# Performance work log

Hardware: AMD Instinct MI355X
Metric: run time of the kernel (lower is better)

The kernel has to match this reference:

```python
import jax, jax.numpy as jnp
import numpy as np

N, F = 4096, 255          # nodes, raw feature dim (one-hot adds +1 -> 256)
HID, D = 256, 256         # GCN hidden and out_dim
B, T, G = 8, 16384, 4     # n_breakings, n_tuples, n_groups
LN_EPS = 1e-5


def setup_inputs() -> dict:
    key = jax.random.key(0)
    ks = jax.random.split(key, 8)
    X = jax.random.normal(ks[0], (N, F), jnp.float32)
    adj_t = jax.random.uniform(ks[1], (N, N), jnp.float32)  # dense weighted adjacency
    W1 = jax.random.normal(ks[2], (F + 1, HID), jnp.float32) * 0.05
    b1 = jnp.zeros((HID,), jnp.float32)
    W2 = jax.random.normal(ks[3], (HID, D), jnp.float32) * 0.05
    b2 = jnp.zeros((D,), jnp.float32)
    ln_gamma = jnp.ones((D,), jnp.float32)
    ln_beta = jnp.zeros((D,), jnp.float32)
    tuples_coo = jax.random.randint(ks[4], (2, T), 0, N)
    group_idx = jax.random.randint(ks[5], (B,), 0, G)
    return dict(X=X, adj_t=adj_t, W1=W1, b1=b1, W2=W2, b2=b2,
                ln_gamma=ln_gamma, ln_beta=ln_beta,
                tuples_coo=tuples_coo, group_idx=group_idx,
                n_breakings=B, n_groups=G)


def reference(X, adj_t, W1, b1, W2, b2, ln_gamma, ln_beta,
              tuples_coo, group_idx, n_breakings, n_groups):
    n = X.shape[0]
    # --- symmetry breaking: top-k degree nodes (ties improbable for float degrees) ---
    deg = adj_t.sum(-1)                                   # [N]
    _, brk_idx = jax.lax.top_k(deg, n_breakings)          # [B]
    one_hot = jax.nn.one_hot(brk_idx, n, dtype=X.dtype)   # [B, N]
    # --- concat broadcast features with one-hot breaking channel ---
    Xin = jnp.concatenate(
        [jnp.broadcast_to(X[None], (n_breakings,) + X.shape), one_hot[..., None]],
        axis=-1)                                          # [B, N, F+1]
    # --- symmetry_breaking_model: 2-layer dense-adjacency GCN ---
    h = jax.nn.relu(jnp.einsum('nm,bmf->bnf', adj_t, Xin) @ W1 + b1)   # [B, N, HID]
    out = jnp.einsum('nm,bmf->bnf', adj_t, h) @ W2 + b2                # [B, N, D]
    # --- LayerNorm over feature dim ---
    mu = out.mean(-1, keepdims=True)
    var = out.var(-1, keepdims=True)
    holo = (out - mu) * jax.lax.rsqrt(var + LN_EPS) * ln_gamma + ln_beta  # [B, N, D]
    # --- gather tuple endpoints and reduce by product over arity ---
    gathered = holo[:, tuples_coo]                        # [B, arity, T, D]
    set_repr = gathered.prod(axis=1)                      # [B, T, D]
    # --- scatter-mean over breakings by group ---
    sums = jax.ops.segment_sum(set_repr, group_idx, num_segments=n_groups)  # [G, T, D]
    counts = jax.ops.segment_sum(jnp.ones((set_repr.shape[0],), set_repr.dtype),
                                 group_idx, num_segments=n_groups)          # [G]
    link = sums / jnp.maximum(counts, 1.0)[:, None, None]  # [G, T, D]
    # transpose(0,1).flatten(1,2): [T, G*D]
    return jnp.transpose(link, (1, 0, 2)).reshape(link.shape[1], -1)
```

## Files before the change

### kernel.cpp

```cpp
#include <hip/hip_runtime.h>
#include <hip/hip_bf16.h>

#define N_NODES 4096
#define FEAT    255
#define NB      8
#define NT      16384
#define NG      4

typedef __attribute__((ext_vector_type(8))) short          short8;
typedef __attribute__((ext_vector_type(8))) __bf16         bf16x8;
typedef __attribute__((ext_vector_type(4))) float          f32x4;
typedef __attribute__((ext_vector_type(4))) unsigned short ushort4v;

__device__ __forceinline__ unsigned short f2bf(float f) {
  unsigned int u = __builtin_bit_cast(unsigned int, f);
  u += 0x7fffu + ((u >> 16) & 1u);
  return (unsigned short)(u >> 16);
}

__device__ __forceinline__ f32x4 mfma16(short8 a, short8 b, f32x4 c) {
  return __builtin_amdgcn_mfma_f32_16x16x32_bf16(
      __builtin_bit_cast(bf16x8, a), __builtin_bit_cast(bf16x8, b), c, 0, 0, 0);
}

__device__ __forceinline__ void gload_lds16(const void* g, void* l) {
  __builtin_amdgcn_global_load_lds((__attribute__((address_space(1))) void*)(void*)g,
                                   (__attribute__((address_space(3))) void*)l, 16, 0, 0);
}

__global__ __launch_bounds__(256)
void deg_cvt(const float* __restrict__ adj, unsigned short* __restrict__ adjbf,
             float* __restrict__ deg)
{
  const int n = blockIdx.x;
  const int tid = threadIdx.x;
  const float* row = adj + (size_t)n * N_NODES;
  float s = 0.f;
#pragma unroll
  for (int it = 0; it < 4; ++it) {
    int idx = it * 1024 + tid * 4;
    float4 v = *(const float4*)(row + idx);
    s += (v.x + v.y) + (v.z + v.w);
    ushort4v o;
    o[0] = f2bf(v.x); o[1] = f2bf(v.y); o[2] = f2bf(v.z); o[3] = f2bf(v.w);
    *(ushort4v*)(adjbf + (size_t)n * N_NODES + idx) = o;
  }
#pragma unroll
  for (int off = 32; off > 0; off >>= 1) s += __shfl_xor(s, off);
  __shared__ float ws4[4];
  if ((tid & 63) == 0) ws4[tid >> 6] = s;
  __syncthreads();
  if (tid == 0) deg[n] = (ws4[0] + ws4[1]) + (ws4[2] + ws4[3]);
}

__global__ __launch_bounds__(256)
void topk_kernel(const float* __restrict__ deg, int* __restrict__ brk)
{
  __shared__ float v[N_NODES];
  __shared__ float wv[4];
  __shared__ int   wi[4];
  const int tid = threadIdx.x;
  for (int i = tid; i < N_NODES; i += 256) v[i] = deg[i];
  __syncthreads();
  for (int it = 0; it < NB; ++it) {
    float best = -1e30f; int bidx = 0x7fffffff;
#pragma unroll
    for (int k = 0; k < N_NODES / 256; ++k) {
      int i = k * 256 + tid;
      float x = v[i];
      if (x > best) { best = x; bidx = i; }
    }
#pragma unroll
    for (int off = 1; off < 64; off <<= 1) {
      float ov = __shfl_xor(best, off);
      int   oi = __shfl_xor(bidx, off);
      if (ov > best || (ov == best && oi < bidx)) { best = ov; bidx = oi; }
    }
    if ((tid & 63) == 0) { wv[tid >> 6] = best; wi[tid >> 6] = bidx; }
    __syncthreads();
    if (tid == 0) {
      float bb = wv[0]; int bbi = wi[0];
#pragma unroll
      for (int k = 1; k < 4; ++k)
        if (wv[k] > bb || (wv[k] == bb && wi[k] < bbi)) { bb = wv[k]; bbi = wi[k]; }
      brk[it] = bbi;
      v[bbi] = -1e30f;
    }
    __syncthreads();
  }
}

#define G0R 8
__global__ __launch_bounds__(256)
void prep_kernel(const float* __restrict__ X, const float* __restrict__ W1,
                 const float* __restrict__ adj, const int* __restrict__ brk,
                 const float* __restrict__ W2,
                 unsigned short* __restrict__ Yt, float* __restrict__ adjcol,
                 unsigned short* __restrict__ W2t)
{
  __shared__ float xr[G0R][256];
  const int bid = blockIdx.x;
  const int tid = threadIdx.x;
  if (bid < 512) {
    const int m0 = bid * G0R;
    for (int i = tid; i < G0R * FEAT; i += 256) {
      int r = i / FEAT, c = i - r * FEAT;
      xr[r][c] = X[(size_t)(m0 + r) * FEAT + c];
    }
    __syncthreads();
    const int d = tid;
    float s[G0R] = {};
    for (int fq = 0; fq < 252; fq += 4) {
      float w0 = W1[(fq + 0) * 256 + d];
      float w1 = W1[(fq + 1) * 256 + d];
      float w2 = W1[(fq + 2) * 256 + d];
      float w3 = W1[(fq + 3) * 256 + d];
#pragma unroll
      for (int r = 0; r < G0R; ++r) {
        float4 x4 = *(const float4*)&xr[r][fq];
        s[r] = fmaf(x4.x, w0, s[r]);
        s[r] = fmaf(x4.y, w1, s[r]);
        s[r] = fmaf(x4.z, w2, s[r]);
        s[r] = fmaf(x4.w, w3, s[r]);
      }
    }
    for (int f = 252; f < FEAT; ++f) {
      float wv = W1[f * 256 + d];
#pragma unroll
      for (int r = 0; r < G0R; ++r) s[r] = fmaf(xr[r][f], wv, s[r]);
    }
#pragma unroll
    for (int r = 0; r < G0R; ++r)
      Yt[(size_t)d * N_NODES + m0 + r] = f2bf(s[r]);
  } else if (bid < 528) {
    const int n = (bid - 512) * 256 + tid;
#pragma unroll
    for (int b = 0; b < NB; ++b)
      adjcol[b * N_NODES + n] = adj[(size_t)n * N_NODES + brk[b]];
  } else {
    const int k = bid - 528, d = tid;
    W2t[(size_t)d * 256 + k] = f2bf(W2[(size_t)k * 256 + d]);
  }
}

template<int BM, int BN, int BK, int FM, int FN, bool OUTBF>
__global__ __launch_bounds__(256)
void gemm_bt(const unsigned short* __restrict__ A, const unsigned short* __restrict__ Bt,
             void* __restrict__ Cv, int M, int Nn, int K)
{
  static_assert(BK == 64, "staging/swizzle math assumes BK=64 (128 B = 8 chunks/row)");
  static_assert(BM == 2 * FM * 16 && BN == 2 * FN * 16, "2x2 wave grid");
  __shared__ unsigned short As[BM * BK];
  __shared__ unsigned short Bs[BN * BK];
  const int tid  = threadIdx.x;
  const int lane = tid & 63;
  const int w    = tid >> 6;
  const int wr   = w >> 1, wc = w & 1;
  const int lhi  = lane >> 4, llo = lane & 15;
  const int brow = blockIdx.x * BM;
  const int bcol = blockIdx.y * BN;
  const int Kper = K / gridDim.z;
  const int kbeg = blockIdx.z * Kper;

  f32x4 acc[FM][FN];
  const f32x4 z = {0.f, 0.f, 0.f, 0.f};
#pragma unroll
  for (int m = 0; m < FM; ++m)
#pragma unroll
    for (int n = 0; n < FN; ++n) acc[m][n] = z;

  for (int k0 = kbeg; k0 < kbeg + Kper; k0 += BK) {
    __syncthreads();
#pragma unroll
    for (int i = 0; i < (BM * BK * 2) / 4096; ++i) {
      int byte = i * 4096 + tid * 16;
      int row  = byte >> 7;
      int sc   = ((byte >> 4) & 7) ^ (row & 7);
      gload_lds16(A + (size_t)(brow + row) * K + k0 + sc * 8,
                  As + ((i * 4096 + w * 1024) >> 1));
    }
#pragma unroll
    for (int i = 0; i < (BN * BK * 2) / 4096; ++i) {
      int byte = i * 4096 + tid * 16;
      int row  = byte >> 7;
      int sc   = ((byte >> 4) & 7) ^ (row & 7);
      gload_lds16(Bt + (size_t)(bcol + row) * K + k0 + sc * 8,
                  Bs + ((i * 4096 + w * 1024) >> 1));
    }
    __syncthreads();
#pragma unroll
    for (int kk = 0; kk < BK; kk += 32) {
      short8 fa[FM], fb[FN];
#pragma unroll
      for (int m = 0; m < FM; ++m) {
        const int ar = wr * FM * 16 + m * 16 + llo;
        const int ac = ((kk >> 3) + lhi) ^ (ar & 7);
        fa[m] = *(const short8*)&As[ar * BK + ac * 8];
      }
#pragma unroll
      for (int n = 0; n < FN; ++n) {
        const int br = wc * FN * 16 + n * 16 + llo;
        const int bc = ((kk >> 3) + lhi) ^ (br & 7);
        fb[n] = *(const short8*)&Bs[br * BK + bc * 8];
      }
#pragma unroll
      for (int m = 0; m < FM; ++m)
#pragma unroll
        for (int n = 0; n < FN; ++n)
          acc[m][n] = mfma16(fa[m], fb[n], acc[m][n]);
    }
  }
#pragma unroll
  for (int m = 0; m < FM; ++m)
#pragma unroll
    for (int n = 0; n < FN; ++n) {
      const int r = brow + wr * FM * 16 + m * 16 + lhi * 4;
      const int c = bcol + wc * FN * 16 + n * 16 + llo;
      if constexpr (OUTBF) {
        unsigned short* cp = (unsigned short*)Cv + (size_t)blockIdx.z * M * Nn
                             + (size_t)r * Nn + c;
#pragma unroll
        for (int i = 0; i < 4; ++i) cp[(size_t)i * Nn] = f2bf(acc[m][n][i]);
      } else {
        float* cp = (float*)Cv + (size_t)blockIdx.z * M * Nn + (size_t)r * Nn + c;
#pragma unroll
        for (int i = 0; i < 4; ++i) cp[(size_t)i * Nn] = acc[m][n][i];
      }
    }
}

__global__ __launch_bounds__(256)
void h_kernel(const float* __restrict__ basep, const float* __restrict__ adjcol,
              const float* __restrict__ b1, const float* __restrict__ W1,
              unsigned short* __restrict__ Ht)
{
  __shared__ float bs[32][261];
  const int tid = threadIdx.x;
  const int m0  = blockIdx.x * 32;
  const int b   = blockIdx.y;
#pragma unroll
  for (int it = 0; it < 8; ++it) {
    int lin = it * 1024 + tid * 4;
    int mm = lin >> 8, d = lin & 255;
    const float* p = basep + (size_t)(m0 + mm) * 256 + d;
    float4 v0 = *(const float4*)(p);
    float4 v1 = *(const float4*)(p + 1048576);
    float4 v2 = *(const float4*)(p + 2097152);
    float4 v3 = *(const float4*)(p + 3145728);
    bs[mm][d]     = ((v0.x + v1.x) + v2.x) + v3.x;
    bs[mm][d + 1] = ((v0.y + v1.y) + v2.y) + v3.y;
    bs[mm][d + 2] = ((v0.z + v1.z) + v2.z) + v3.z;
    bs[mm][d + 3] = ((v0.w + v1.w) + v2.w) + v3.w;
  }
  __syncthreads();
  const int ml = tid & 31, dg = tid >> 5;
  const float ac = adjcol[b * N_NODES + m0 + ml];
  const float* w1l = W1 + 255 * 256;
#pragma unroll 4
  for (int dd = 0; dd < 32; ++dd) {
    int d = dg * 32 + dd;
    float v = bs[ml][d] + b1[d] + ac * w1l[d];
    v = fmaxf(v, 0.f);
    Ht[(size_t)(b * 256 + d) * N_NODES + m0 + ml] = f2bf(v);
  }
}

__global__ __launch_bounds__(256)
void gemm3_ln(const unsigned short* __restrict__ Mcat, const unsigned short* __restrict__ W2t,
              const float* __restrict__ b2, const float* __restrict__ gamma,
              const float* __restrict__ beta, float* __restrict__ holo)
{
  const int tid  = threadIdx.x;
  const int w    = tid >> 6, lane = tid & 63;
  const int lhi  = lane >> 4, llo = lane & 15;
  const int n0   = blockIdx.x * 64;
  const int b    = blockIdx.y;
  const int row0 = n0 + w * 16;

  f32x4 acc[16];
  const f32x4 z = {0.f, 0.f, 0.f, 0.f};
#pragma unroll
  for (int j = 0; j < 16; ++j) acc[j] = z;

  const unsigned short* arow = Mcat + (size_t)(row0 + llo) * 2048 + b * 256;
#pragma unroll
  for (int k0 = 0; k0 < 256; k0 += 32) {
    const short8 fa = *(const short8*)&arow[k0 + lhi * 8];
#pragma unroll
    for (int j = 0; j < 16; ++j) {
      const short8 fb = *(const short8*)&W2t[(size_t)(j * 16 + llo) * 256 + k0 + lhi * 8];
      acc[j] = mfma16(fa, fb, acc[j]);
    }
  }
  float b2v[16];
#pragma unroll
  for (int j = 0; j < 16; ++j) b2v[j] = b2[j * 16 + llo];

  float mu[4], rs[4];
#pragma unroll
  for (int i = 0; i < 4; ++i) {
    float s = 0.f;
#pragma unroll
    for (int j = 0; j < 16; ++j) s += acc[j][i] + b2v[j];
    s += __shfl_xor(s, 1); s += __shfl_xor(s, 2);
    s += __shfl_xor(s, 4); s += __shfl_xor(s, 8);
    mu[i] = s * (1.f / 256.f);
  }
#pragma unroll
  for (int i = 0; i < 4; ++i) {
    float q = 0.f;
#pragma unroll
    for (int j = 0; j < 16; ++j) { float d = acc[j][i] + b2v[j] - mu[i]; q += d * d; }
    q += __shfl_xor(q, 1); q += __shfl_xor(q, 2);
    q += __shfl_xor(q, 4); q += __shfl_xor(q, 8);
    rs[i] = rsqrtf(q * (1.f / 256.f) + 1e-5f);
  }
  float* hb = holo + ((size_t)(row0 + lhi * 4) * 8 + b) * 256 + llo;
#pragma unroll
  for (int j = 0; j < 16; ++j) {
    const float gv = gamma[j * 16 + llo];
    const float bt = beta[j * 16 + llo];
#pragma unroll
    for (int i = 0; i < 4; ++i) {
      float x = acc[j][i] + b2v[j];
      hb[(size_t)i * 2048 + j * 16] = (x - mu[i]) * rs[i] * gv + bt;
    }
  }
}

__global__ __launch_bounds__(256)
void gather_k(const float* __restrict__ holo, const int* __restrict__ tc,
              const int* __restrict__ gidx, float* __restrict__ out)
{
  const int t = blockIdx.x;
  const int d = threadIdx.x;
  const int i = tc[t];
  const int j = tc[NT + t];
  const float* hi = holo + (size_t)i * 2048 + d;
  const float* hj = holo + (size_t)j * 2048 + d;
  float a0 = 0.f, a1 = 0.f, a2 = 0.f, a3 = 0.f;
  float c0 = 0.f, c1 = 0.f, c2 = 0.f, c3 = 0.f;
#pragma unroll
  for (int b = 0; b < NB; ++b) {
    const int g = gidx[b];
    const float p = hi[b * 256] * hj[b * 256];
    a0 += (g == 0) ? p : 0.f;  c0 += (g == 0) ? 1.f : 0.f;
    a1 += (g == 1) ? p : 0.f;  c1 += (g == 1) ? 1.f : 0.f;
    a2 += (g == 2) ? p : 0.f;  c2 += (g == 2) ? 1.f : 0.f;
    a3 += (g == 3) ? p : 0.f;  c3 += (g == 3) ? 1.f : 0.f;
  }
  float* ob = out + (size_t)t * 1024 + d;
  ob[0]   = a0 / fmaxf(c0, 1.f);
  ob[256] = a1 / fmaxf(c1, 1.f);
  ob[512] = a2 / fmaxf(c2, 1.f);
  ob[768] = a3 / fmaxf(c3, 1.f);
}

extern "C" void kernel_launch(void* const* d_in, const int* in_sizes, int n_in,
                              void* d_out, int out_size, void* d_ws, size_t ws_size,
                              hipStream_t stream)
{
  const float* X     = (const float*)d_in[0];
  const float* adj   = (const float*)d_in[1];
  const float* W1    = (const float*)d_in[2];
  const float* b1    = (const float*)d_in[3];
  const float* W2    = (const float*)d_in[4];
  const float* b2    = (const float*)d_in[5];
  const float* gamma = (const float*)d_in[6];
  const float* beta  = (const float*)d_in[7];
  const int*   tc    = (const int*)d_in[8];
  const int*   gidx  = (const int*)d_in[9];

  char* w = (char*)d_ws;
  size_t off = 0;
  unsigned short* adjbf = (unsigned short*)(w + off);
  float*          holo  = (float*)(w + off);  off += 33554432;
  unsigned short* Ht    = (unsigned short*)(w + off); off += 16777216;
  unsigned short* Mcat  = (unsigned short*)(w + off); off += 16777216;
  float*          basep = (float*)(w + off);  off += 16777216;
  unsigned short* Yt    = (unsigned short*)(w + off); off += 2097152;
  float*          deg   = (float*)(w + off);  off += 16384;
  int*            brk   = (int*)(w + off);    off += 256;
  float*          adjcol= (float*)(w + off);  off += 131072;
  unsigned short* W2t   = (unsigned short*)(w + off); off += 131072;
  float* out = (float*)d_out;

  deg_cvt     <<<N_NODES, 256, 0, stream>>>(adj, adjbf, deg);
  topk_kernel <<<1, 256, 0, stream>>>(deg, brk);
  prep_kernel <<<784, 256, 0, stream>>>(X, W1, adj, brk, W2, Yt, adjcol, W2t);
  gemm_bt<64, 128, 64, 2, 4, false><<<dim3(N_NODES / 64, 256 / 128, 4), 256, 0, stream>>>(
      adjbf, Yt, basep, N_NODES, 256, N_NODES);
  h_kernel    <<<dim3(N_NODES / 32, NB), 256, 0, stream>>>(basep, adjcol, b1, W1, Ht);
  gemm_bt<128, 128, 64, 4, 4, true><<<dim3(N_NODES / 128, 2048 / 128, 1), 256, 0, stream>>>(
      adjbf, Ht, Mcat, N_NODES, 2048, N_NODES);
  gemm3_ln    <<<dim3(N_NODES / 64, NB), 256, 0, stream>>>(Mcat, W2t, b2, gamma, beta, holo);
  gather_k    <<<NT, 256, 0, stream>>>(holo, tc, gidx, out);
}
```

Measured before the change: 362.6 us.

## Store second GEMM output per-breaking, stage A tile in LDS, widen h_kernel and gather blocks

The bf16 output of the big adjacency GEMM now goes to a [B][N][256] layout instead of [N][2048]. gemm3_ln can then load its 64x256 A tile contiguously into LDS with a swizzle through async global-to-LDS loads, rather than reading strided rows straight from global memory. h_kernel is retiled to 128 nodes by 32-feature chunks across a z grid dimension, so the transposed Ht writes are more coalesced. gather_k handles four tuples per block and keeps group indices in registers. The new layout's stores span 256-element rows, which may change write efficiency in the GEMM epilogue, and the added LDS per block may reduce occupancy.

```diff
diff --git a/kernel.cpp b/kernel.cpp
--- a/kernel.cpp
+++ b/kernel.cpp
@@ -217,10 +217,10 @@
       const int r = brow + wr * FM * 16 + m * 16 + lhi * 4;
       const int c = bcol + wc * FN * 16 + n * 16 + llo;
       if constexpr (OUTBF) {
-        unsigned short* cp = (unsigned short*)Cv + (size_t)blockIdx.z * M * Nn
-                             + (size_t)r * Nn + c;
-#pragma unroll
-        for (int i = 0; i < 4; ++i) cp[(size_t)i * Nn] = f2bf(acc[m][n][i]);
+        unsigned short* Cb = (unsigned short*)Cv;
+        const size_t base = ((size_t)(c >> 8) * M) * 256 + (c & 255);
+#pragma unroll
+        for (int i = 0; i < 4; ++i) Cb[base + (size_t)(r + i) * 256] = f2bf(acc[m][n][i]);
       } else {
         float* cp = (float*)Cv + (size_t)blockIdx.z * M * Nn + (size_t)r * Nn + c;
 #pragma unroll
@@ -234,42 +234,49 @@
               const float* __restrict__ b1, const float* __restrict__ W1,
               unsigned short* __restrict__ Ht)
 {
-  __shared__ float bs[32][261];
-  const int tid = threadIdx.x;
-  const int m0  = blockIdx.x * 32;
-  const int b   = blockIdx.y;
-#pragma unroll
-  for (int it = 0; it < 8; ++it) {
-    int lin = it * 1024 + tid * 4;
-    int mm = lin >> 8, d = lin & 255;
-    const float* p = basep + (size_t)(m0 + mm) * 256 + d;
-    float4 v0 = *(const float4*)(p);
-    float4 v1 = *(const float4*)(p + 1048576);
-    float4 v2 = *(const float4*)(p + 2097152);
-    float4 v3 = *(const float4*)(p + 3145728);
-    bs[mm][d]     = ((v0.x + v1.x) + v2.x) + v3.x;
-    bs[mm][d + 1] = ((v0.y + v1.y) + v2.y) + v3.y;
-    bs[mm][d + 2] = ((v0.z + v1.z) + v2.z) + v3.z;
-    bs[mm][d + 3] = ((v0.w + v1.w) + v2.w) + v3.w;
-  }
-  __syncthreads();
-  const int ml = tid & 31, dg = tid >> 5;
+  __shared__ float bs[128][33];
+  const int tid  = threadIdx.x;
+  const int m0   = blockIdx.x * 128;
+  const int b    = blockIdx.y;
+  const int dh   = blockIdx.z;
+  const int ml   = tid & 127, half = tid >> 7;
   const float ac = adjcol[b * N_NODES + m0 + ml];
   const float* w1l = W1 + 255 * 256;
-#pragma unroll 4
-  for (int dd = 0; dd < 32; ++dd) {
-    int d = dg * 32 + dd;
-    float v = bs[ml][d] + b1[d] + ac * w1l[d];
-    v = fmaxf(v, 0.f);
-    Ht[(size_t)(b * 256 + d) * N_NODES + m0 + ml] = f2bf(v);
-  }
-}
-
-__global__ __launch_bounds__(256)
-void gemm3_ln(const unsigned short* __restrict__ Mcat, const unsigned short* __restrict__ W2t,
+  for (int c = 0; c < 4; ++c) {
+    const int d0 = (dh * 4 + c) * 32;
+    __syncthreads();
+#pragma unroll
+    for (int it = 0; it < 4; ++it) {
+      int li = it * 256 + tid;
+      int m = li >> 3, q = li & 7;
+      const float* p = basep + (size_t)(m0 + m) * 256 + d0 + q * 4;
+      float4 v0 = *(const float4*)(p);
+      float4 v1 = *(const float4*)(p + 1048576);
+      float4 v2 = *(const float4*)(p + 2097152);
+      float4 v3 = *(const float4*)(p + 3145728);
+      bs[m][q * 4 + 0] = ((v0.x + v1.x) + v2.x) + v3.x;
+      bs[m][q * 4 + 1] = ((v0.y + v1.y) + v2.y) + v3.y;
+      bs[m][q * 4 + 2] = ((v0.z + v1.z) + v2.z) + v3.z;
+      bs[m][q * 4 + 3] = ((v0.w + v1.w) + v2.w) + v3.w;
+    }
+    __syncthreads();
+#pragma unroll
+    for (int k = 0; k < 16; ++k) {
+      int dd = half * 16 + k;
+      int d  = d0 + dd;
+      float v = bs[ml][dd] + b1[d] + ac * w1l[d];
+      v = fmaxf(v, 0.f);
+      Ht[(size_t)(b * 256 + d) * N_NODES + m0 + ml] = f2bf(v);
+    }
+  }
+}
+
+__global__ __launch_bounds__(256)
+void gemm3_ln(const unsigned short* __restrict__ Mcat2, const unsigned short* __restrict__ W2t,
               const float* __restrict__ b2, const float* __restrict__ gamma,
               const float* __restrict__ beta, float* __restrict__ holo)
 {
+  __shared__ unsigned short As[64 * 256];
   const int tid  = threadIdx.x;
   const int w    = tid >> 6, lane = tid & 63;
   const int lhi  = lane >> 4, llo = lane & 15;
@@ -277,15 +284,26 @@
   const int b    = blockIdx.y;
   const int row0 = n0 + w * 16;
 
+#pragma unroll
+  for (int i = 0; i < 8; ++i) {
+    int byte = i * 4096 + tid * 16;
+    int row  = byte >> 9;
+    int sc   = ((byte >> 4) & 31) ^ (row & 7);
+    gload_lds16(Mcat2 + ((size_t)b * N_NODES + n0 + row) * 256 + sc * 8,
+                As + ((i * 4096 + w * 1024) >> 1));
+  }
+  __syncthreads();
+
   f32x4 acc[16];
   const f32x4 z = {0.f, 0.f, 0.f, 0.f};
 #pragma unroll
   for (int j = 0; j < 16; ++j) acc[j] = z;
 
-  const unsigned short* arow = Mcat + (size_t)(row0 + llo) * 2048 + b * 256;
+  const int ar = w * 16 + llo;
 #pragma unroll
   for (int k0 = 0; k0 < 256; k0 += 32) {
-    const short8 fa = *(const short8*)&arow[k0 + lhi * 8];
+    const int ac = ((k0 >> 3) + lhi) ^ (ar & 7);
+    const short8 fa = *(const short8*)&As[ar * 256 + ac * 8];
 #pragma unroll
     for (int j = 0; j < 16; ++j) {
       const short8 fb = *(const short8*)&W2t[(size_t)(j * 16 + llo) * 256 + k0 + lhi * 8];
@@ -332,28 +350,34 @@
 void gather_k(const float* __restrict__ holo, const int* __restrict__ tc,
               const int* __restrict__ gidx, float* __restrict__ out)
 {
-  const int t = blockIdx.x;
-  const int d = threadIdx.x;
-  const int i = tc[t];
-  const int j = tc[NT + t];
-  const float* hi = holo + (size_t)i * 2048 + d;
-  const float* hj = holo + (size_t)j * 2048 + d;
-  float a0 = 0.f, a1 = 0.f, a2 = 0.f, a3 = 0.f;
-  float c0 = 0.f, c1 = 0.f, c2 = 0.f, c3 = 0.f;
-#pragma unroll
-  for (int b = 0; b < NB; ++b) {
-    const int g = gidx[b];
-    const float p = hi[b * 256] * hj[b * 256];
-    a0 += (g == 0) ? p : 0.f;  c0 += (g == 0) ? 1.f : 0.f;
-    a1 += (g == 1) ? p : 0.f;  c1 += (g == 1) ? 1.f : 0.f;
-    a2 += (g == 2) ? p : 0.f;  c2 += (g == 2) ? 1.f : 0.f;
-    a3 += (g == 3) ? p : 0.f;  c3 += (g == 3) ? 1.f : 0.f;
-  }
-  float* ob = out + (size_t)t * 1024 + d;
-  ob[0]   = a0 / fmaxf(c0, 1.f);
-  ob[256] = a1 / fmaxf(c1, 1.f);
-  ob[512] = a2 / fmaxf(c2, 1.f);
-  ob[768] = a3 / fmaxf(c3, 1.f);
+  const int t0 = blockIdx.x * 4;
+  const int d  = threadIdx.x;
+  int g[NB];
+#pragma unroll
+  for (int b = 0; b < NB; ++b) g[b] = gidx[b];
+#pragma unroll
+  for (int tt = 0; tt < 4; ++tt) {
+    const int t = t0 + tt;
+    const int i = tc[t];
+    const int j = tc[NT + t];
+    const float* hi = holo + (size_t)i * 2048 + d;
+    const float* hj = holo + (size_t)j * 2048 + d;
+    float a0 = 0.f, a1 = 0.f, a2 = 0.f, a3 = 0.f;
+    float c0 = 0.f, c1 = 0.f, c2 = 0.f, c3 = 0.f;
+#pragma unroll
+    for (int b = 0; b < NB; ++b) {
+      const float p = hi[b * 256] * hj[b * 256];
+      a0 += (g[b] == 0) ? p : 0.f;  c0 += (g[b] == 0) ? 1.f : 0.f;
+      a1 += (g[b] == 1) ? p : 0.f;  c1 += (g[b] == 1) ? 1.f : 0.f;
+      a2 += (g[b] == 2) ? p : 0.f;  c2 += (g[b] == 2) ? 1.f : 0.f;
+      a3 += (g[b] == 3) ? p : 0.f;  c3 += (g[b] == 3) ? 1.f : 0.f;
+    }
+    float* ob = out + (size_t)t * 1024 + d;
+    ob[0]   = a0 / fmaxf(c0, 1.f);
+    ob[256] = a1 / fmaxf(c1, 1.f);
+    ob[512] = a2 / fmaxf(c2, 1.f);
+    ob[768] = a3 / fmaxf(c3, 1.f);
+  }
 }
 
 extern "C" void kernel_launch(void* const* d_in, const int* in_sizes, int n_in,
@@ -376,7 +400,7 @@
   unsigned short* adjbf = (unsigned short*)(w + off);
   float*          holo  = (float*)(w + off);  off += 33554432;
   unsigned short* Ht    = (unsigned short*)(w + off); off += 16777216;
-  unsigned short* Mcat  = (unsigned short*)(w + off); off += 16777216;
+  unsigned short* Mcat2 = (unsigned short*)(w + off); off += 16777216;
   float*          basep = (float*)(w + off);  off += 16777216;
   unsigned short* Yt    = (unsigned short*)(w + off); off += 2097152;
   float*          deg   = (float*)(w + off);  off += 16384;
@@ -390,9 +414,9 @@
   prep_kernel <<<784, 256, 0, stream>>>(X, W1, adj, brk, W2, Yt, adjcol, W2t);
   gemm_bt<64, 128, 64, 2, 4, false><<<dim3(N_NODES / 64, 256 / 128, 4), 256, 0, stream>>>(
       adjbf, Yt, basep, N_NODES, 256, N_NODES);
-  h_kernel    <<<dim3(N_NODES / 32, NB), 256, 0, stream>>>(basep, adjcol, b1, W1, Ht);
+  h_kernel    <<<dim3(N_NODES / 128, NB, 2), 256, 0, stream>>>(basep, adjcol, b1, W1, Ht);
   gemm_bt<128, 128, 64, 4, 4, true><<<dim3(N_NODES / 128, 2048 / 128, 1), 256, 0, stream>>>(
-      adjbf, Ht, Mcat, N_NODES, 2048, N_NODES);
-  gemm3_ln    <<<dim3(N_NODES / 64, NB), 256, 0, stream>>>(Mcat, W2t, b2, gamma, beta, holo);
-  gather_k    <<<NT, 256, 0, stream>>>(holo, tc, gidx, out);
-}
+      adjbf, Ht, Mcat2, N_NODES, 2048, N_NODES);
+  gemm3_ln    <<<dim3(N_NODES / 64, NB), 256, 0, stream>>>(Mcat2, W2t, b2, gamma, beta, holo);
+  gather_k    <<<NT / 4, 256, 0, stream>>>(holo, tc, gidx, out);
+}
```

After: 367.9 us. Within noise of the previous version (+1.5%).
